# Performance work log

Measured on AMD Instinct MI355X. Metric: run time of the kernel, lower is better.

Reference implementation:

```python
import jax, jax.numpy as jnp
import numpy as np

B, S, E, H, STEPS = 32, 2048, 300, 256, 24


def setup_inputs() -> dict:
    key = jax.random.key(0)
    ks = jax.random.split(key, 16)
    sc = 0.05
    inp = {
        "input_ids": jax.random.normal(ks[0], (B, S, E), dtype=jnp.float32),
        "tree_ids": jax.random.randint(ks[1], (B, STEPS, S), 0, S),
        "tree_ids_r": jax.random.randint(ks[2], (B, STEPS, S), 0, S),
        "tree_ids_l": jax.random.randint(ks[3], (B, STEPS, S), 0, S),
        # N-ary (binary) TreeLSTM parameters (Tai et al. 2015)
        "W_iou": jax.random.normal(ks[4], (E, 3 * H), dtype=jnp.float32) * sc,
        "b_iou": jnp.zeros((3 * H,), dtype=jnp.float32),
        "U_iou_l": jax.random.normal(ks[5], (H, 3 * H), dtype=jnp.float32) * sc,
        "U_iou_r": jax.random.normal(ks[6], (H, 3 * H), dtype=jnp.float32) * sc,
        "W_f": jax.random.normal(ks[7], (E, H), dtype=jnp.float32) * sc,
        "b_f": jnp.zeros((H,), dtype=jnp.float32),
        "U_f_ll": jax.random.normal(ks[8], (H, H), dtype=jnp.float32) * sc,
        "U_f_lr": jax.random.normal(ks[9], (H, H), dtype=jnp.float32) * sc,
        "U_f_rl": jax.random.normal(ks[10], (H, H), dtype=jnp.float32) * sc,
        "U_f_rr": jax.random.normal(ks[11], (H, H), dtype=jnp.float32) * sc,
    }
    return inp


def _gather_nodes(t, idx):
    # t: [B,S,H], idx: [B,S] -> [B,S,H]
    return jnp.take_along_axis(t, idx[..., None], axis=1)


def reference(input_ids, tree_ids, tree_ids_r, tree_ids_l,
              W_iou, b_iou, U_iou_l, U_iou_r,
              W_f, b_f, U_f_ll, U_f_lr, U_f_rl, U_f_rr):
    dt = input_ids.dtype
    h0 = jnp.zeros((B, S, H), dtype=dt)
    c0 = jnp.zeros((B, S, H), dtype=dt)
    # input projections are step-invariant: compute once
    x_iou = input_ids @ W_iou + b_iou          # [B,S,3H]
    x_f = input_ids @ W_f + b_f                # [B,S,H]
    bidx = jnp.arange(B)[:, None]              # [B,1]

    def step(carry, ids):
        h, c = carry
        idd, idl, idr = ids                    # each [B,S]
        h_l = _gather_nodes(h, idl); c_l = _gather_nodes(c, idl)
        h_r = _gather_nodes(h, idr); c_r = _gather_nodes(c, idr)
        iou = x_iou + h_l @ U_iou_l + h_r @ U_iou_r
        i, o, u = jnp.split(iou, 3, axis=-1)
        i = jax.nn.sigmoid(i); o = jax.nn.sigmoid(o); u = jnp.tanh(u)
        f_l = jax.nn.sigmoid(x_f + h_l @ U_f_ll + h_r @ U_f_lr)
        f_r = jax.nn.sigmoid(x_f + h_l @ U_f_rl + h_r @ U_f_rr)
        c_new = i * u + f_l * c_l + f_r * c_r
        h_new = o * jnp.tanh(c_new)
        # scatter updates to destination node ids; slot 0 is the null slot
        h = h.at[bidx, idd].set(h_new)
        c = c.at[bidx, idd].set(c_new)
        h = h.at[:, 0].set(0.0)
        c = c.at[:, 0].set(0.0)
        return (h, c), None

    ids_seq = (jnp.transpose(tree_ids, (1, 0, 2)),
               jnp.transpose(tree_ids_l, (1, 0, 2)),
               jnp.transpose(tree_ids_r, (1, 0, 2)))
    (h, c), _ = jax.lax.scan(step, (h0, c0), ids_seq)

    roots = tree_ids[:, -1, :].max(axis=1)     # [B]
    h_root = jnp.take_along_axis(
        h, jnp.broadcast_to(roots[:, None, None], (B, 1, H)), axis=1)[:, 0]
    return (h, c, h_root)
```

## Files before the change

kernel.cpp:

```cpp
#include <hip/hip_runtime.h>
#include <hip/hip_bf16.h>
#include <math.h>

#define B_     32
#define S_     2048
#define E_     300
#define H_     256
#define STEPS_ 24
#define BS_    (B_ * S_)
#define NPACK  1280
#define KSL    16
#define KSLP   10
#define COPYB  1024

typedef __bf16 bf16x8 __attribute__((ext_vector_type(8)));
typedef float  f32x4  __attribute__((ext_vector_type(4)));

__device__ __forceinline__ float sigm(float x) {
    return 1.0f / (1.0f + __expf(-x));
}
__device__ __forceinline__ float fast_tanh(float x) {
    return 2.0f * sigm(2.0f * x) - 1.0f;
}
__device__ __forceinline__ float bf16bits2f(unsigned short u) {
    return __uint_as_float(((unsigned)u) << 16);
}
__device__ __forceinline__ void gload_lds16(const void* g, void* l) {
    __builtin_amdgcn_global_load_lds(
        (const __attribute__((address_space(1))) void*)g,
        (__attribute__((address_space(3))) void*)l, 16, 0, 0);
}

__global__ __launch_bounds__(256) void pack_B_kernel(
    const float* __restrict__ U_iou_l, const float* __restrict__ U_iou_r,
    const float* __restrict__ U_f_ll,  const float* __restrict__ U_f_lr,
    const float* __restrict__ U_f_rl,  const float* __restrict__ U_f_rr,
    __hip_bfloat16* __restrict__ Bp)
{
    const int idx = blockIdx.x * 256 + threadIdx.x;
    if (idx >= KSL * NPACK * 32) return;
    const int ks = idx / (NPACK * 32);
    const int rem = idx - ks * (NPACK * 32);
    const int p = rem >> 5;
    const int kin = rem & 31;
    const int k = ks * 32 + kin;
    const int w = p / 80;
    const int rg = p - w * 80;
    const int g = rg >> 4;
    const int c = w * 16 + (rg & 15);
    float v;
    if (g < 3) {
        const int col = g * 256 + c;
        v = (k < 256) ? U_iou_l[k * 768 + col] : U_iou_r[(k - 256) * 768 + col];
    } else if (g == 3) {
        v = (k < 256) ? U_f_ll[k * 256 + c] : U_f_lr[(k - 256) * 256 + c];
    } else {
        v = (k < 256) ? U_f_rl[k * 256 + c] : U_f_rr[(k - 256) * 256 + c];
    }
    Bp[idx] = __float2bfloat16(v);
}

__global__ __launch_bounds__(256) void pack_W_kernel(
    const float* __restrict__ W_iou, const float* __restrict__ W_f,
    __hip_bfloat16* __restrict__ Wp)
{
    const int idx = blockIdx.x * 256 + threadIdx.x;
    if (idx >= KSLP * 1024 * 32) return;
    const int ks = idx / (1024 * 32);
    const int rem = idx - ks * (1024 * 32);
    const int p = rem >> 5;
    const int kin = rem & 31;
    const int k = ks * 32 + kin;
    const int cw = p >> 6;
    const int g = (p >> 4) & 3;
    const int col = cw * 16 + (p & 15);
    float v = 0.f;
    if (k < E_) v = (g < 3) ? W_iou[k * 768 + g * 256 + col] : W_f[k * 256 + col];
    Wp[idx] = __float2bfloat16(v);
}

__global__ __launch_bounds__(256) void winner_kernel(
    const int* __restrict__ tree_ids, int* __restrict__ winner)
{
    const int idx = blockIdx.x * 256 + threadIdx.x;
    if (idx >= B_ * STEPS_ * S_) return;
    const int b = idx / (STEPS_ * S_);
    const int rem = idx - b * (STEPS_ * S_);
    const int t = rem / S_;
    const int s = rem - t * S_;
    const int d = tree_ids[idx];
    if ((unsigned)d < (unsigned)S_)
        atomicMax(&winner[(size_t)t * BS_ + b * S_ + d], s);
}

__global__ __launch_bounds__(256) void compact_kernel(
    const int* __restrict__ winner, int* __restrict__ compact,
    int* __restrict__ count)
{
    const int tb = blockIdx.x;
    const int tid = threadIdx.x;
    const int* w = winner + (size_t)tb * S_;
    int* cmp = compact + (size_t)tb * S_;
    __shared__ int scan_[256];
    __shared__ int base_;
    if (tid == 0) base_ = 0;
    __syncthreads();
    for (int chunk = 0; chunk < S_ / 256; ++chunk) {
        const int d = chunk * 256 + tid;
        const int s = w[d];
        const int p = (d != 0 && s >= 0) ? 1 : 0;
        int v = p;
        scan_[tid] = v;
        __syncthreads();
        for (int off = 1; off < 256; off <<= 1) {
            const int add = (tid >= off) ? scan_[tid - off] : 0;
            __syncthreads();
            v += add;
            scan_[tid] = v;
            __syncthreads();
        }
        const int mybase = base_;
        if (p) cmp[mybase + v - 1] = (s << 11) | d;
        __syncthreads();
        if (tid == 0) base_ += scan_[255];
        __syncthreads();
    }
    if (tid == 0) count[tb] = base_;
}

__global__ __launch_bounds__(256, 3) void proj_kernel(
    const float* __restrict__ input, const __hip_bfloat16* __restrict__ Wp,
    const float* __restrict__ b_iou, const float* __restrict__ b_f,
    __hip_bfloat16* __restrict__ x_pack)
{
    __shared__ __hip_bfloat16 Ash[64][328];
    const int tid = threadIdx.x;
    const int grp = blockIdx.x >> 5;
    const int l32 = blockIdx.x & 31;
    const int cb  = l32 >> 3;
    const int rg  = grp * 8 + (l32 & 7);
    const int row0 = rg * 64;

    for (int it = 0; it < 20; ++it) {
        const int idx = tid + it * 256;
        const int r = idx / 80;
        const int c4 = idx - r * 80;
        float4 v = make_float4(0.f, 0.f, 0.f, 0.f);
        if (c4 < 75) v = *(const float4*)(input + (size_t)(row0 + r) * E_ + c4 * 4);
        union { __hip_bfloat16 h[4]; uint2 u; } tconv;
        tconv.h[0] = __float2bfloat16(v.x);
        tconv.h[1] = __float2bfloat16(v.y);
        tconv.h[2] = __float2bfloat16(v.z);
        tconv.h[3] = __float2bfloat16(v.w);
        *(uint2*)&Ash[r][c4 * 4] = tconv.u;
    }
    __syncthreads();

    const int lane = tid & 63;
    const int wave = tid >> 6;
    const int m16 = lane & 15;
    const int q = lane >> 4;
    const int chunk = cb * 4 + wave;
    const int c = chunk * 16 + m16;

    f32x4 acc[4][4];
    const f32x4 z4 = {0.f, 0.f, 0.f, 0.f};
#pragma unroll
    for (int s = 0; s < 4; ++s)
#pragma unroll
        for (int g = 0; g < 4; ++g) acc[s][g] = z4;

    const __hip_bfloat16* wpb = Wp + ((size_t)(chunk * 64 + m16)) * 32 + q * 8;
    for (int ks = 0; ks < KSLP; ++ks) {
        bf16x8 bfrag[4];
#pragma unroll
        for (int g = 0; g < 4; ++g)
            bfrag[g] = *reinterpret_cast<const bf16x8*>(wpb + (size_t)ks * 32768 + g * 512);
        bf16x8 a[4];
#pragma unroll
        for (int s = 0; s < 4; ++s)
            a[s] = *reinterpret_cast<const bf16x8*>(&Ash[s * 16 + m16][ks * 32 + q * 8]);
#pragma unroll
        for (int s = 0; s < 4; ++s)
#pragma unroll
            for (int g = 0; g < 4; ++g)
                acc[s][g] = __builtin_amdgcn_mfma_f32_16x16x32_bf16(a[s], bfrag[g], acc[s][g], 0, 0, 0);
    }

    const float bi0 = b_iou[c];
    const float bi1 = b_iou[256 + c];
    const float bi2 = b_iou[512 + c];
    const float bf_ = b_f[c];
#pragma unroll
    for (int s = 0; s < 4; ++s) {
#pragma unroll
        for (int j = 0; j < 4; ++j) {
            const int row = row0 + s * 16 + q * 4 + j;
            const size_t xrow = (size_t)row * 1024;
            union { __hip_bfloat16 h[4]; uint2 u; } pk;
            pk.h[0] = __float2bfloat16(acc[s][0][j] + bi0);
            pk.h[1] = __float2bfloat16(acc[s][1][j] + bi1);
            pk.h[2] = __float2bfloat16(acc[s][2][j] + bi2);
            pk.h[3] = __float2bfloat16(acc[s][3][j] + bf_);
            *(uint2*)(x_pack + xrow + (size_t)c * 4) = pk.u;
        }
    }
}

__global__ __launch_bounds__(256, 4) void step_kernel(
    const __hip_bfloat16* __restrict__ h_cur, const __hip_bfloat16* __restrict__ c_cur,
    __hip_bfloat16* __restrict__ h_next, __hip_bfloat16* __restrict__ c_next,
    const int* __restrict__ tree_ids_l, const int* __restrict__ tree_ids_r,
    const int* __restrict__ winner_t, const int* __restrict__ compact,
    const int* __restrict__ count, const __hip_bfloat16* __restrict__ x_pack,
    const __hip_bfloat16* __restrict__ Bp, int t)
{
    const int tid = threadIdx.x;

    if (blockIdx.x < COPYB) {
        const uint4* h_cur4 = (const uint4*)h_cur;
        const uint4* c_cur4 = (const uint4*)c_cur;
        uint4* h_next4 = (uint4*)h_next;
        uint4* c_next4 = (uint4*)c_next;
#pragma unroll
        for (int i = 0; i < 8; ++i) {
            const int idx = blockIdx.x * 256 + tid + i * (COPYB * 256);
            const int row = idx >> 5;
            const int d = row & (S_ - 1);
            if (d == 0) {
                const uint4 z = make_uint4(0u, 0u, 0u, 0u);
                h_next4[idx] = z;
                c_next4[idx] = z;
            } else if (winner_t[row] < 0) {
                h_next4[idx] = h_cur4[idx];
                c_next4[idx] = c_cur4[idx];
            }
        }
        return;
    }

    const int sb     = blockIdx.x - COPYB;
    const int grp    = sb >> 5;
    const int l32    = sb & 31;
    const int nq     = l32 >> 3;
    const int tile_g = grp * 8 + (l32 & 7);
    const int b    = tile_g >> 6;
    const int tile = tile_g & 63;
    const int nAct = count[t * B_ + b];
    const int s0 = tile * 32;
    if (s0 >= nAct) return;

    __shared__ __hip_bfloat16 Ash[32][520];
    __shared__ int sS[32], sD[32], sIdl[32], sIdr[32];

    const int* cmp = compact + ((size_t)(t * B_ + b)) * S_;
    if (tid < 32) {
        const int gi = s0 + tid;
        const int pair = (gi < nAct) ? cmp[gi] : 0;
        sS[tid] = pair >> 11;
        sD[tid] = pair & 2047;
    }
    __syncthreads();

    const int lane = tid & 63;
    const int wave = tid >> 6;
    const int m16 = lane & 15;
    const int q = lane >> 4;
    const int w16 = nq * 4 + wave;
    const int cg = w16 * 16 + m16;

    uint2 xv[2][4];
#pragma unroll
    for (int sm = 0; sm < 2; ++sm)
#pragma unroll
        for (int j = 0; j < 4; ++j) {
            const int r = sm * 16 + q * 4 + j;
            xv[sm][j] = *(const uint2*)(x_pack
                + ((size_t)(b * S_ + sS[r])) * 1024 + (size_t)cg * 4);
        }

    const int* idl_b = tree_ids_l + ((size_t)b * STEPS_ + t) * S_;
    const int* idr_b = tree_ids_r + ((size_t)b * STEPS_ + t) * S_;
    if (tid < 32)       sIdl[tid]      = idl_b[sS[tid]];
    else if (tid < 64)  sIdr[tid - 32] = idr_b[sS[tid - 32]];
    __syncthreads();

    unsigned short clb[2][4], crb[2][4];
    const __hip_bfloat16* cbase = c_cur + (size_t)(b * S_) * H_ + cg;
#pragma unroll
    for (int sm = 0; sm < 2; ++sm)
#pragma unroll
        for (int j = 0; j < 4; ++j) {
            const int r = sm * 16 + q * 4 + j;
            clb[sm][j] = *(const unsigned short*)(cbase + (size_t)sIdl[r] * H_);
            crb[sm][j] = *(const unsigned short*)(cbase + (size_t)sIdr[r] * H_);
        }

    {
        const int half = lane >> 5;
        const int c16 = lane & 31;
#pragma unroll
        for (int it = 0; it < 8; ++it) {
            const int r = wave + it * 4;
            const int src = half ? sIdr[r] : sIdl[r];
            const __hip_bfloat16* g =
                h_cur + ((size_t)(b * S_) + src) * H_ + c16 * 8;
            gload_lds16(g, &Ash[r][0]);
        }
    }
    __syncthreads();

    f32x4 acc[2][5];
    const f32x4 z4 = {0.f, 0.f, 0.f, 0.f};
#pragma unroll
    for (int sm = 0; sm < 2; ++sm)
#pragma unroll
        for (int g = 0; g < 5; ++g) acc[sm][g] = z4;

    const __hip_bfloat16* bp_base =
        Bp + ((size_t)(w16 * 80 + m16)) * 32 + q * 8;

    for (int ks = 0; ks < KSL; ++ks) {
        const bf16x8 a0 = *reinterpret_cast<const bf16x8*>(&Ash[m16][ks * 32 + q * 8]);
        const bf16x8 a1 = *reinterpret_cast<const bf16x8*>(&Ash[16 + m16][ks * 32 + q * 8]);
        const __hip_bfloat16* bk = bp_base + (size_t)ks * (NPACK * 32);
        bf16x8 bfrag[5];
#pragma unroll
        for (int g = 0; g < 5; ++g)
            bfrag[g] = *reinterpret_cast<const bf16x8*>(bk + g * 512);
#pragma unroll
        for (int g = 0; g < 5; ++g) {
            acc[0][g] = __builtin_amdgcn_mfma_f32_16x16x32_bf16(a0, bfrag[g], acc[0][g], 0, 0, 0);
            acc[1][g] = __builtin_amdgcn_mfma_f32_16x16x32_bf16(a1, bfrag[g], acc[1][g], 0, 0, 0);
        }
    }

#pragma unroll
    for (int sm = 0; sm < 2; ++sm) {
#pragma unroll
        for (int j = 0; j < 4; ++j) {
            const int r = sm * 16 + q * 4 + j;
            const int d = sD[r];
            if (d == 0) continue;
            const size_t orow = ((size_t)(b * S_ + d)) * H_;
            union { uint2 u; unsigned short x[4]; } xu;
            xu.u = xv[sm][j];
            const float xi = bf16bits2f(xu.x[0]);
            const float xo = bf16bits2f(xu.x[1]);
            const float xuu = bf16bits2f(xu.x[2]);
            const float xf = bf16bits2f(xu.x[3]);
            const float ig = sigm(acc[sm][0][j] + xi);
            const float og = sigm(acc[sm][1][j] + xo);
            const float ug = fast_tanh(acc[sm][2][j] + xuu);
            const float fl = sigm(acc[sm][3][j] + xf);
            const float fr = sigm(acc[sm][4][j] + xf);
            const float cl = bf16bits2f(clb[sm][j]);
            const float cr = bf16bits2f(crb[sm][j]);
            const float cn = ig * ug + fl * cl + fr * cr;
            const float hn = og * fast_tanh(cn);
            c_next[orow + cg] = __float2bfloat16(cn);
            h_next[orow + cg] = __float2bfloat16(hn);
        }
    }
}

__global__ __launch_bounds__(256) void convert_kernel(
    const __hip_bfloat16* __restrict__ h, const __hip_bfloat16* __restrict__ c,
    float* __restrict__ out_h, float* __restrict__ out_c)
{
    const size_t i = ((size_t)blockIdx.x * 256 + threadIdx.x) * 8;
#pragma unroll
    for (int j = 0; j < 8; ++j) {
        out_h[i + j] = __bfloat162float(h[i + j]);
        out_c[i + j] = __bfloat162float(c[i + j]);
    }
}

__global__ __launch_bounds__(256) void root_kernel(
    const int* __restrict__ tree_ids,
    const __hip_bfloat16* __restrict__ h, float* __restrict__ h_root)
{
    const int b = blockIdx.x;
    const int tid = threadIdx.x;
    const int* ids = tree_ids + ((size_t)b * STEPS_ + (STEPS_ - 1)) * S_;
    __shared__ int red[256];
    int m = 0;
    for (int s = tid; s < S_; s += 256) m = max(m, ids[s]);
    red[tid] = m;
    __syncthreads();
    for (int off = 128; off > 0; off >>= 1) {
        if (tid < off) red[tid] = max(red[tid], red[tid + off]);
        __syncthreads();
    }
    const int root = red[0];
    h_root[(size_t)b * H_ + tid] =
        __bfloat162float(h[((size_t)(b * S_) + root) * H_ + tid]);
}

extern "C" void kernel_launch(void* const* d_in, const int* in_sizes, int n_in,
                              void* d_out, int out_size, void* d_ws, size_t ws_size,
                              hipStream_t stream)
{
    const float* input_ids  = (const float*)d_in[0];
    const int*   tree_ids   = (const int*)d_in[1];
    const int*   tree_ids_r = (const int*)d_in[2];
    const int*   tree_ids_l = (const int*)d_in[3];
    const float* W_iou   = (const float*)d_in[4];
    const float* b_iou   = (const float*)d_in[5];
    const float* U_iou_l = (const float*)d_in[6];
    const float* U_iou_r = (const float*)d_in[7];
    const float* W_f     = (const float*)d_in[8];
    const float* b_f     = (const float*)d_in[9];
    const float* U_f_ll  = (const float*)d_in[10];
    const float* U_f_lr  = (const float*)d_in[11];
    const float* U_f_rl  = (const float*)d_in[12];
    const float* U_f_rr  = (const float*)d_in[13];

    float* out = (float*)d_out;
    float* out_h = out;
    float* out_c = out + (size_t)BS_ * H_;
    float* out_root = out + (size_t)2 * BS_ * H_;

    char* ws = (char*)d_ws;
    __hip_bfloat16* x_pack = (__hip_bfloat16*)(ws);
    __hip_bfloat16* hA     = (__hip_bfloat16*)(ws + 134217728ull);
    __hip_bfloat16* cA     = (__hip_bfloat16*)(ws + 167772160ull);
    int*            winner = (int*)(ws + 201326592ull);
    __hip_bfloat16* Bp     = (__hip_bfloat16*)(ws + 207618048ull);
    __hip_bfloat16* Wp     = (__hip_bfloat16*)(ws + 208928768ull);
    __hip_bfloat16* hB     = (__hip_bfloat16*)out_h;
    __hip_bfloat16* cB     = (__hip_bfloat16*)out_c;
    int* compact = (int*)((char*)out_h + 33554432ull);
    int* cnt     = compact + (size_t)STEPS_ * B_ * S_;

    hipMemsetAsync(hA, 0, (size_t)BS_ * H_ * sizeof(__hip_bfloat16), stream);
    hipMemsetAsync(cA, 0, (size_t)BS_ * H_ * sizeof(__hip_bfloat16), stream);
    hipMemsetAsync(winner, 0xFF, (size_t)STEPS_ * BS_ * sizeof(int), stream);

    pack_B_kernel<<<(KSL * NPACK * 32 + 255) / 256, 256, 0, stream>>>(
        U_iou_l, U_iou_r, U_f_ll, U_f_lr, U_f_rl, U_f_rr, Bp);
    pack_W_kernel<<<(KSLP * 1024 * 32 + 255) / 256, 256, 0, stream>>>(W_iou, W_f, Wp);
    winner_kernel<<<(B_ * STEPS_ * S_) / 256, 256, 0, stream>>>(tree_ids, winner);
    compact_kernel<<<STEPS_ * B_, 256, 0, stream>>>(winner, compact, cnt);
    proj_kernel<<<(BS_ / 64) * 4, 256, 0, stream>>>(input_ids, Wp, b_iou, b_f, x_pack);

    for (int t = 0; t < STEPS_; ++t) {
        const __hip_bfloat16* hc = (t & 1) ? hB : hA;
        const __hip_bfloat16* cc = (t & 1) ? cB : cA;
        __hip_bfloat16*       hn = (t & 1) ? hA : hB;
        __hip_bfloat16*       cn = (t & 1) ? cA : cB;
        const int* wt = winner + (size_t)t * BS_;

        step_kernel<<<COPYB + B_ * 64 * 4, 256, 0, stream>>>(
            hc, cc, hn, cn, tree_ids_l, tree_ids_r, wt,
            compact, cnt, x_pack, Bp, t);
    }

    convert_kernel<<<(BS_ * H_ / 8) / 256, 256, 0, stream>>>(hA, cA, out_h, out_c);
    root_kernel<<<B_, 256, 0, stream>>>(tree_ids, hA, out_root);
}
```

Before: 4.326 ms.

## Fuse input projection into step kernel, computing only for active rows

```diff
diff --git a/kernel.cpp b/kernel.cpp
--- a/kernel.cpp
+++ b/kernel.cpp
@@ -10,7 +10,7 @@
 #define BS_    (B_ * S_)
 #define NPACK  1280
 #define KSL    16
-#define KSLP   10
+#define KSL2   10
 #define COPYB  1024
 
 typedef __bf16 bf16x8 __attribute__((ext_vector_type(8)));
@@ -60,23 +60,40 @@
     Bp[idx] = __float2bfloat16(v);
 }
 
-__global__ __launch_bounds__(256) void pack_W_kernel(
+__global__ __launch_bounds__(256) void pack_B2_kernel(
     const float* __restrict__ W_iou, const float* __restrict__ W_f,
-    __hip_bfloat16* __restrict__ Wp)
+    __hip_bfloat16* __restrict__ B2)
 {
     const int idx = blockIdx.x * 256 + threadIdx.x;
-    if (idx >= KSLP * 1024 * 32) return;
-    const int ks = idx / (1024 * 32);
-    const int rem = idx - ks * (1024 * 32);
+    if (idx >= KSL2 * NPACK * 32) return;
+    const int ks = idx / (NPACK * 32);
+    const int rem = idx - ks * (NPACK * 32);
     const int p = rem >> 5;
     const int kin = rem & 31;
     const int k = ks * 32 + kin;
-    const int cw = p >> 6;
-    const int g = (p >> 4) & 3;
-    const int col = cw * 16 + (p & 15);
+    const int w = p / 80;
+    const int rg = p - w * 80;
+    const int g = rg >> 4;
+    const int c = w * 16 + (rg & 15);
     float v = 0.f;
-    if (k < E_) v = (g < 3) ? W_iou[k * 768 + g * 256 + col] : W_f[k * 256 + col];
-    Wp[idx] = __float2bfloat16(v);
+    if (k < E_) v = (g < 3) ? W_iou[k * 768 + g * 256 + c] : W_f[k * 256 + c];
+    B2[idx] = __float2bfloat16(v);
+}
+
+__global__ __launch_bounds__(256) void inpcvt_kernel(
+    const float* __restrict__ in, __hip_bfloat16* __restrict__ out)
+{
+    const int idx = blockIdx.x * 256 + threadIdx.x;
+    const int row = idx >> 6;
+    const int c0 = (idx & 63) * 8;
+    union { __hip_bfloat16 h[8]; uint4 u; } o;
+#pragma unroll
+    for (int j = 0; j < 8; ++j) {
+        const int c = c0 + j;
+        o.h[j] = (c < E_) ? __float2bfloat16(in[(size_t)row * E_ + c])
+                          : __float2bfloat16(0.f);
+    }
+    *(uint4*)(out + (size_t)row * 512 + c0) = o.u;
 }
 
 __global__ __launch_bounds__(256) void winner_kernel(
@@ -128,92 +145,15 @@
     if (tid == 0) count[tb] = base_;
 }
 
-__global__ __launch_bounds__(256, 3) void proj_kernel(
-    const float* __restrict__ input, const __hip_bfloat16* __restrict__ Wp,
-    const float* __restrict__ b_iou, const float* __restrict__ b_f,
-    __hip_bfloat16* __restrict__ x_pack)
-{
-    __shared__ __hip_bfloat16 Ash[64][328];
-    const int tid = threadIdx.x;
-    const int grp = blockIdx.x >> 5;
-    const int l32 = blockIdx.x & 31;
-    const int cb  = l32 >> 3;
-    const int rg  = grp * 8 + (l32 & 7);
-    const int row0 = rg * 64;
-
-    for (int it = 0; it < 20; ++it) {
-        const int idx = tid + it * 256;
-        const int r = idx / 80;
-        const int c4 = idx - r * 80;
-        float4 v = make_float4(0.f, 0.f, 0.f, 0.f);
-        if (c4 < 75) v = *(const float4*)(input + (size_t)(row0 + r) * E_ + c4 * 4);
-        union { __hip_bfloat16 h[4]; uint2 u; } tconv;
-        tconv.h[0] = __float2bfloat16(v.x);
-        tconv.h[1] = __float2bfloat16(v.y);
-        tconv.h[2] = __float2bfloat16(v.z);
-        tconv.h[3] = __float2bfloat16(v.w);
-        *(uint2*)&Ash[r][c4 * 4] = tconv.u;
-    }
-    __syncthreads();
-
-    const int lane = tid & 63;
-    const int wave = tid >> 6;
-    const int m16 = lane & 15;
-    const int q = lane >> 4;
-    const int chunk = cb * 4 + wave;
-    const int c = chunk * 16 + m16;
-
-    f32x4 acc[4][4];
-    const f32x4 z4 = {0.f, 0.f, 0.f, 0.f};
-#pragma unroll
-    for (int s = 0; s < 4; ++s)
-#pragma unroll
-        for (int g = 0; g < 4; ++g) acc[s][g] = z4;
-
-    const __hip_bfloat16* wpb = Wp + ((size_t)(chunk * 64 + m16)) * 32 + q * 8;
-    for (int ks = 0; ks < KSLP; ++ks) {
-        bf16x8 bfrag[4];
-#pragma unroll
-        for (int g = 0; g < 4; ++g)
-            bfrag[g] = *reinterpret_cast<const bf16x8*>(wpb + (size_t)ks * 32768 + g * 512);
-        bf16x8 a[4];
-#pragma unroll
-        for (int s = 0; s < 4; ++s)
-            a[s] = *reinterpret_cast<const bf16x8*>(&Ash[s * 16 + m16][ks * 32 + q * 8]);
-#pragma unroll
-        for (int s = 0; s < 4; ++s)
-#pragma unroll
-            for (int g = 0; g < 4; ++g)
-                acc[s][g] = __builtin_amdgcn_mfma_f32_16x16x32_bf16(a[s], bfrag[g], acc[s][g], 0, 0, 0);
-    }
-
-    const float bi0 = b_iou[c];
-    const float bi1 = b_iou[256 + c];
-    const float bi2 = b_iou[512 + c];
-    const float bf_ = b_f[c];
-#pragma unroll
-    for (int s = 0; s < 4; ++s) {
-#pragma unroll
-        for (int j = 0; j < 4; ++j) {
-            const int row = row0 + s * 16 + q * 4 + j;
-            const size_t xrow = (size_t)row * 1024;
-            union { __hip_bfloat16 h[4]; uint2 u; } pk;
-            pk.h[0] = __float2bfloat16(acc[s][0][j] + bi0);
-            pk.h[1] = __float2bfloat16(acc[s][1][j] + bi1);
-            pk.h[2] = __float2bfloat16(acc[s][2][j] + bi2);
-            pk.h[3] = __float2bfloat16(acc[s][3][j] + bf_);
-            *(uint2*)(x_pack + xrow + (size_t)c * 4) = pk.u;
-        }
-    }
-}
-
 __global__ __launch_bounds__(256, 4) void step_kernel(
     const __hip_bfloat16* __restrict__ h_cur, const __hip_bfloat16* __restrict__ c_cur,
     __hip_bfloat16* __restrict__ h_next, __hip_bfloat16* __restrict__ c_next,
     const int* __restrict__ tree_ids_l, const int* __restrict__ tree_ids_r,
     const int* __restrict__ winner_t, const int* __restrict__ compact,
-    const int* __restrict__ count, const __hip_bfloat16* __restrict__ x_pack,
-    const __hip_bfloat16* __restrict__ Bp, int t)
+    const int* __restrict__ count, const __hip_bfloat16* __restrict__ inp,
+    const float* __restrict__ b_iou, const float* __restrict__ b_f,
+    const __hip_bfloat16* __restrict__ Bp, const __hip_bfloat16* __restrict__ B2,
+    int t)
 {
     const int tid = threadIdx.x;
 
@@ -269,15 +209,10 @@
     const int w16 = nq * 4 + wave;
     const int cg = w16 * 16 + m16;
 
-    uint2 xv[2][4];
-#pragma unroll
-    for (int sm = 0; sm < 2; ++sm)
-#pragma unroll
-        for (int j = 0; j < 4; ++j) {
-            const int r = sm * 16 + q * 4 + j;
-            xv[sm][j] = *(const uint2*)(x_pack
-                + ((size_t)(b * S_ + sS[r])) * 1024 + (size_t)cg * 4);
-        }
+    const float bi0 = b_iou[cg];
+    const float bi1 = b_iou[256 + cg];
+    const float bi2 = b_iou[512 + cg];
+    const float bfv = b_f[cg];
 
     const int* idl_b = tree_ids_l + ((size_t)b * STEPS_ + t) * S_;
     const int* idr_b = tree_ids_r + ((size_t)b * STEPS_ + t) * S_;
@@ -334,6 +269,36 @@
             acc[1][g] = __builtin_amdgcn_mfma_f32_16x16x32_bf16(a1, bfrag[g], acc[1][g], 0, 0, 0);
         }
     }
+    __syncthreads();
+
+    {
+#pragma unroll
+        for (int it = 0; it < 8; ++it) {
+            const int r = wave + it * 4;
+            const __hip_bfloat16* g =
+                inp + ((size_t)(b * S_) + sS[r]) * 512 + lane * 8;
+            gload_lds16(g, &Ash[r][0]);
+        }
+    }
+    __syncthreads();
+
+    const __hip_bfloat16* b2_base =
+        B2 + ((size_t)(w16 * 80 + m16)) * 32 + q * 8;
+
+    for (int ks = 0; ks < KSL2; ++ks) {
+        const bf16x8 a0 = *reinterpret_cast<const bf16x8*>(&Ash[m16][ks * 32 + q * 8]);
+        const bf16x8 a1 = *reinterpret_cast<const bf16x8*>(&Ash[16 + m16][ks * 32 + q * 8]);
+        const __hip_bfloat16* bk = b2_base + (size_t)ks * (NPACK * 32);
+        bf16x8 bfrag[5];
+#pragma unroll
+        for (int g = 0; g < 5; ++g)
+            bfrag[g] = *reinterpret_cast<const bf16x8*>(bk + g * 512);
+#pragma unroll
+        for (int g = 0; g < 5; ++g) {
+            acc[0][g] = __builtin_amdgcn_mfma_f32_16x16x32_bf16(a0, bfrag[g], acc[0][g], 0, 0, 0);
+            acc[1][g] = __builtin_amdgcn_mfma_f32_16x16x32_bf16(a1, bfrag[g], acc[1][g], 0, 0, 0);
+        }
+    }
 
 #pragma unroll
     for (int sm = 0; sm < 2; ++sm) {
@@ -343,17 +308,11 @@
             const int d = sD[r];
             if (d == 0) continue;
             const size_t orow = ((size_t)(b * S_ + d)) * H_;
-            union { uint2 u; unsigned short x[4]; } xu;
-            xu.u = xv[sm][j];
-            const float xi = bf16bits2f(xu.x[0]);
-            const float xo = bf16bits2f(xu.x[1]);
-            const float xuu = bf16bits2f(xu.x[2]);
-            const float xf = bf16bits2f(xu.x[3]);
-            const float ig = sigm(acc[sm][0][j] + xi);
-            const float og = sigm(acc[sm][1][j] + xo);
-            const float ug = fast_tanh(acc[sm][2][j] + xuu);
-            const float fl = sigm(acc[sm][3][j] + xf);
-            const float fr = sigm(acc[sm][4][j] + xf);
+            const float ig = sigm(acc[0][0][j * 0 + 0] * 0.f + acc[sm][0][j] + bi0);
+            const float og = sigm(acc[sm][1][j] + bi1);
+            const float ug = fast_tanh(acc[sm][2][j] + bi2);
+            const float fl = sigm(acc[sm][3][j] + bfv);
+            const float fr = sigm(acc[sm][4][j] + bfv);
             const float cl = bf16bits2f(clb[sm][j]);
             const float cr = bf16bits2f(crb[sm][j]);
             const float cn = ig * ug + fl * cl + fr * cr;
@@ -422,12 +381,12 @@
     float* out_root = out + (size_t)2 * BS_ * H_;
 
     char* ws = (char*)d_ws;
-    __hip_bfloat16* x_pack = (__hip_bfloat16*)(ws);
+    __hip_bfloat16* inp_bf = (__hip_bfloat16*)(ws);
+    __hip_bfloat16* B2     = (__hip_bfloat16*)(ws + 67108864ull);
     __hip_bfloat16* hA     = (__hip_bfloat16*)(ws + 134217728ull);
     __hip_bfloat16* cA     = (__hip_bfloat16*)(ws + 167772160ull);
     int*            winner = (int*)(ws + 201326592ull);
     __hip_bfloat16* Bp     = (__hip_bfloat16*)(ws + 207618048ull);
-    __hip_bfloat16* Wp     = (__hip_bfloat16*)(ws + 208928768ull);
     __hip_bfloat16* hB     = (__hip_bfloat16*)out_h;
     __hip_bfloat16* cB     = (__hip_bfloat16*)out_c;
     int* compact = (int*)((char*)out_h + 33554432ull);
@@ -439,10 +398,11 @@
 
     pack_B_kernel<<<(KSL * NPACK * 32 + 255) / 256, 256, 0, stream>>>(
         U_iou_l, U_iou_r, U_f_ll, U_f_lr, U_f_rl, U_f_rr, Bp);
-    pack_W_kernel<<<(KSLP * 1024 * 32 + 255) / 256, 256, 0, stream>>>(W_iou, W_f, Wp);
+    pack_B2_kernel<<<(KSL2 * NPACK * 32 + 255) / 256, 256, 0, stream>>>(
+        W_iou, W_f, B2);
     winner_kernel<<<(B_ * STEPS_ * S_) / 256, 256, 0, stream>>>(tree_ids, winner);
     compact_kernel<<<STEPS_ * B_, 256, 0, stream>>>(winner, compact, cnt);
-    proj_kernel<<<(BS_ / 64) * 4, 256, 0, stream>>>(input_ids, Wp, b_iou, b_f, x_pack);
+    inpcvt_kernel<<<(BS_ * 64) / 256, 256, 0, stream>>>(input_ids, inp_bf);
 
     for (int t = 0; t < STEPS_; ++t) {
         const __hip_bfloat16* hc = (t & 1) ? hB : hA;
@@ -453,7 +413,7 @@
 
         step_kernel<<<COPYB + B_ * 64 * 4, 256, 0, stream>>>(
             hc, cc, hn, cn, tree_ids_l, tree_ids_r, wt,
-            compact, cnt, x_pack, Bp, t);
+            compact, cnt, inp_bf, b_iou, b_f, Bp, B2, t);
     }
 
     convert_kernel<<<(BS_ * H_ / 8) / 256, 256, 0, stream>>>(hA, cA, out_h, out_c);
```

After: 5.756 ms. +33.1%, slower.

## Replace per-step state copies with per-row epoch ping-pong buffers

Applied to the files above, without the earlier changes.

```diff
diff --git a/kernel.cpp b/kernel.cpp
--- a/kernel.cpp
+++ b/kernel.cpp
@@ -11,7 +11,6 @@
 #define NPACK  1280
 #define KSL    16
 #define KSLP   10
-#define COPYB  1024
 
 typedef __bf16 bf16x8 __attribute__((ext_vector_type(8)));
 typedef float  f32x4  __attribute__((ext_vector_type(4)));
@@ -93,11 +92,47 @@
         atomicMax(&winner[(size_t)t * BS_ + b * S_ + d], s);
 }
 
+__global__ __launch_bounds__(256) void epoch_kernel(
+    const int* __restrict__ winner, unsigned* __restrict__ ep)
+{
+    const int r = blockIdx.x * 256 + threadIdx.x;
+    if (r >= BS_) return;
+    const int d = r & (S_ - 1);
+    unsigned bits = 0;
+    int e = 0;
+    for (int t = 0; t < STEPS_; ++t) {
+        bits |= (unsigned)e << t;
+        if (d != 0 && winner[(size_t)t * BS_ + r] >= 0) e ^= 1;
+    }
+    bits |= (unsigned)e << STEPS_;
+    ep[r] = bits;
+}
+
+__global__ __launch_bounds__(256) void aug_kernel(
+    const int* __restrict__ tree_ids_l, const int* __restrict__ tree_ids_r,
+    const unsigned* __restrict__ ep,
+    int* __restrict__ aug_l, int* __restrict__ aug_r)
+{
+    const int idx = blockIdx.x * 256 + threadIdx.x;
+    if (idx >= B_ * STEPS_ * S_) return;
+    const int b = idx / (STEPS_ * S_);
+    const int rem = idx - b * (STEPS_ * S_);
+    const int t = rem / S_;
+    const int vl = tree_ids_l[idx];
+    const int vr = tree_ids_r[idx];
+    const int bl = (ep[b * S_ + vl] >> t) & 1;
+    const int br = (ep[b * S_ + vr] >> t) & 1;
+    aug_l[idx] = vl | (bl << 11);
+    aug_r[idx] = vr | (br << 11);
+}
+
 __global__ __launch_bounds__(256) void compact_kernel(
-    const int* __restrict__ winner, int* __restrict__ compact,
-    int* __restrict__ count)
+    const int* __restrict__ winner, const unsigned* __restrict__ ep,
+    int* __restrict__ compact, int* __restrict__ count)
 {
     const int tb = blockIdx.x;
+    const int t_ = tb / B_;
+    const int b_ = tb - t_ * B_;
     const int tid = threadIdx.x;
     const int* w = winner + (size_t)tb * S_;
     int* cmp = compact + (size_t)tb * S_;
@@ -120,7 +155,10 @@
             __syncthreads();
         }
         const int mybase = base_;
-        if (p) cmp[mybase + v - 1] = (s << 11) | d;
+        if (p) {
+            const int wb = (ep[b_ * S_ + d] >> (t_ + 1)) & 1;
+            cmp[mybase + v - 1] = (s << 11) | d | (wb << 22);
+        }
         __syncthreads();
         if (tid == 0) base_ += scan_[255];
         __syncthreads();
@@ -208,38 +246,15 @@
 }
 
 __global__ __launch_bounds__(256, 4) void step_kernel(
-    const __hip_bfloat16* __restrict__ h_cur, const __hip_bfloat16* __restrict__ c_cur,
-    __hip_bfloat16* __restrict__ h_next, __hip_bfloat16* __restrict__ c_next,
-    const int* __restrict__ tree_ids_l, const int* __restrict__ tree_ids_r,
-    const int* __restrict__ winner_t, const int* __restrict__ compact,
-    const int* __restrict__ count, const __hip_bfloat16* __restrict__ x_pack,
+    __hip_bfloat16* __restrict__ h0, __hip_bfloat16* __restrict__ c0,
+    __hip_bfloat16* __restrict__ h1, __hip_bfloat16* __restrict__ c1,
+    const int* __restrict__ aug_l, const int* __restrict__ aug_r,
+    const int* __restrict__ compact, const int* __restrict__ count,
+    const __hip_bfloat16* __restrict__ x_pack,
     const __hip_bfloat16* __restrict__ Bp, int t)
 {
     const int tid = threadIdx.x;
-
-    if (blockIdx.x < COPYB) {
-        const uint4* h_cur4 = (const uint4*)h_cur;
-        const uint4* c_cur4 = (const uint4*)c_cur;
-        uint4* h_next4 = (uint4*)h_next;
-        uint4* c_next4 = (uint4*)c_next;
-#pragma unroll
-        for (int i = 0; i < 8; ++i) {
-            const int idx = blockIdx.x * 256 + tid + i * (COPYB * 256);
-            const int row = idx >> 5;
-            const int d = row & (S_ - 1);
-            if (d == 0) {
-                const uint4 z = make_uint4(0u, 0u, 0u, 0u);
-                h_next4[idx] = z;
-                c_next4[idx] = z;
-            } else if (winner_t[row] < 0) {
-                h_next4[idx] = h_cur4[idx];
-                c_next4[idx] = c_cur4[idx];
-            }
-        }
-        return;
-    }
-
-    const int sb     = blockIdx.x - COPYB;
+    const int sb     = blockIdx.x;
     const int grp    = sb >> 5;
     const int l32    = sb & 31;
     const int nq     = l32 >> 3;
@@ -251,14 +266,15 @@
     if (s0 >= nAct) return;
 
     __shared__ __hip_bfloat16 Ash[32][520];
-    __shared__ int sS[32], sD[32], sIdl[32], sIdr[32];
+    __shared__ int sS[32], sD[32], sW[32], sIdl[32], sIdr[32];
 
     const int* cmp = compact + ((size_t)(t * B_ + b)) * S_;
     if (tid < 32) {
         const int gi = s0 + tid;
         const int pair = (gi < nAct) ? cmp[gi] : 0;
-        sS[tid] = pair >> 11;
+        sS[tid] = (pair >> 11) & 2047;
         sD[tid] = pair & 2047;
+        sW[tid] = (pair >> 22) & 1;
     }
     __syncthreads();
 
@@ -279,21 +295,26 @@
                 + ((size_t)(b * S_ + sS[r])) * 1024 + (size_t)cg * 4);
         }
 
-    const int* idl_b = tree_ids_l + ((size_t)b * STEPS_ + t) * S_;
-    const int* idr_b = tree_ids_r + ((size_t)b * STEPS_ + t) * S_;
+    const int* idl_b = aug_l + ((size_t)b * STEPS_ + t) * S_;
+    const int* idr_b = aug_r + ((size_t)b * STEPS_ + t) * S_;
     if (tid < 32)       sIdl[tid]      = idl_b[sS[tid]];
     else if (tid < 64)  sIdr[tid - 32] = idr_b[sS[tid - 32]];
     __syncthreads();
 
     unsigned short clb[2][4], crb[2][4];
-    const __hip_bfloat16* cbase = c_cur + (size_t)(b * S_) * H_ + cg;
 #pragma unroll
     for (int sm = 0; sm < 2; ++sm)
 #pragma unroll
         for (int j = 0; j < 4; ++j) {
             const int r = sm * 16 + q * 4 + j;
-            clb[sm][j] = *(const unsigned short*)(cbase + (size_t)sIdl[r] * H_);
-            crb[sm][j] = *(const unsigned short*)(cbase + (size_t)sIdr[r] * H_);
+            const int vl = sIdl[r];
+            const int vr = sIdr[r];
+            const __hip_bfloat16* cl_ = (vl >> 11) ? c1 : c0;
+            const __hip_bfloat16* cr_ = (vr >> 11) ? c1 : c0;
+            clb[sm][j] = *(const unsigned short*)(
+                cl_ + ((size_t)(b * S_) + (vl & 2047)) * H_ + cg);
+            crb[sm][j] = *(const unsigned short*)(
+                cr_ + ((size_t)(b * S_) + (vr & 2047)) * H_ + cg);
         }
 
     {
@@ -302,9 +323,10 @@
 #pragma unroll
         for (int it = 0; it < 8; ++it) {
             const int r = wave + it * 4;
-            const int src = half ? sIdr[r] : sIdl[r];
+            const int v = half ? sIdr[r] : sIdl[r];
+            const __hip_bfloat16* hb = (v >> 11) ? h1 : h0;
             const __hip_bfloat16* g =
-                h_cur + ((size_t)(b * S_) + src) * H_ + c16 * 8;
+                hb + ((size_t)(b * S_) + (v & 2047)) * H_ + c16 * 8;
             gload_lds16(g, &Ash[r][0]);
         }
     }
@@ -358,9 +380,24 @@
             const float cr = bf16bits2f(crb[sm][j]);
             const float cn = ig * ug + fl * cl + fr * cr;
             const float hn = og * fast_tanh(cn);
-            c_next[orow + cg] = __float2bfloat16(cn);
-            h_next[orow + cg] = __float2bfloat16(hn);
-        }
+            __hip_bfloat16* hd = sW[r] ? h1 : h0;
+            __hip_bfloat16* cd = sW[r] ? c1 : c0;
+            cd[orow + cg] = __float2bfloat16(cn);
+            hd[orow + cg] = __float2bfloat16(hn);
+        }
+    }
+}
+
+__global__ __launch_bounds__(256) void consolidate_kernel(
+    const unsigned* __restrict__ ep,
+    const uint4* __restrict__ h1, uint4* __restrict__ h0,
+    const uint4* __restrict__ c1, uint4* __restrict__ c0)
+{
+    const int idx = blockIdx.x * 256 + threadIdx.x;
+    const int row = idx >> 5;
+    if ((ep[row] >> STEPS_) & 1) {
+        h0[idx] = h1[idx];
+        c0[idx] = c1[idx];
     }
 }
 
@@ -432,6 +469,9 @@
     __hip_bfloat16* cB     = (__hip_bfloat16*)out_c;
     int* compact = (int*)((char*)out_h + 33554432ull);
     int* cnt     = compact + (size_t)STEPS_ * B_ * S_;
+    int* aug_l   = (int*)((char*)out_c + 33554432ull);
+    int* aug_r   = aug_l + (size_t)B_ * STEPS_ * S_;
+    unsigned* ep = (unsigned*)(aug_r + (size_t)B_ * STEPS_ * S_);
 
     hipMemsetAsync(hA, 0, (size_t)BS_ * H_ * sizeof(__hip_bfloat16), stream);
     hipMemsetAsync(cA, 0, (size_t)BS_ * H_ * sizeof(__hip_bfloat16), stream);
@@ -441,21 +481,19 @@
         U_iou_l, U_iou_r, U_f_ll, U_f_lr, U_f_rl, U_f_rr, Bp);
     pack_W_kernel<<<(KSLP * 1024 * 32 + 255) / 256, 256, 0, stream>>>(W_iou, W_f, Wp);
     winner_kernel<<<(B_ * STEPS_ * S_) / 256, 256, 0, stream>>>(tree_ids, winner);
-    compact_kernel<<<STEPS_ * B_, 256, 0, stream>>>(winner, compact, cnt);
+    epoch_kernel<<<BS_ / 256, 256, 0, stream>>>(winner, ep);
+    compact_kernel<<<STEPS_ * B_, 256, 0, stream>>>(winner, ep, compact, cnt);
+    aug_kernel<<<(B_ * STEPS_ * S_) / 256, 256, 0, stream>>>(
+        tree_ids_l, tree_ids_r, ep, aug_l, aug_r);
     proj_kernel<<<(BS_ / 64) * 4, 256, 0, stream>>>(input_ids, Wp, b_iou, b_f, x_pack);
 
     for (int t = 0; t < STEPS_; ++t) {
-        const __hip_bfloat16* hc = (t & 1) ? hB : hA;
-        const __hip_bfloat16* cc = (t & 1) ? cB : cA;
-        __hip_bfloat16*       hn = (t & 1) ? hA : hB;
-        __hip_bfloat16*       cn = (t & 1) ? cA : cB;
-        const int* wt = winner + (size_t)t * BS_;
-
-        step_kernel<<<COPYB + B_ * 64 * 4, 256, 0, stream>>>(
-            hc, cc, hn, cn, tree_ids_l, tree_ids_r, wt,
-            compact, cnt, x_pack, Bp, t);
-    }
-
+        step_kernel<<<B_ * 64 * 4, 256, 0, stream>>>(
+            hA, cA, hB, cB, aug_l, aug_r, compact, cnt, x_pack, Bp, t);
+    }
+
+    consolidate_kernel<<<(BS_ * 32) / 256, 256, 0, stream>>>(
+        ep, (const uint4*)hB, (uint4*)hA, (const uint4*)cB, (uint4*)cA);
     convert_kernel<<<(BS_ * H_ / 8) / 256, 256, 0, stream>>>(hA, cA, out_h, out_c);
     root_kernel<<<B_, 256, 0, stream>>>(tree_ids, hA, out_root);
 }
```

After: 4.226 ms. 2.3% less time.
